# Kernel tuning notes

Hardware: AMD Instinct MI355X
Metric: run time of the kernel (lower is better)

The kernel has to match this reference:

```python
import jax, jax.numpy as jnp
import numpy as np

W_BITS = 4  # active precision (max of supported_bits)
EPS = 0.005  # clamp margin from the original module


def _dequant_kbit(qweight, lut, w_bits):
    """Bit-plane LUT dequant.
    qweight: [w_bits, O, I//32] int32, plane b holds bit b (MSB-first code) of each
    weight's k-bit index, 32 consecutive input positions per int32 word (LSB-first
    within a word). lut: [O, 2**w_bits]. Returns dense weight [O, I].
    """
    O = qweight.shape[1]
    shifts = jnp.arange(32, dtype=jnp.int32)                     # bit position within word
    bits = (qweight[:, :, :, None] >> shifts) & 1                # [w_bits, O, I//32, 32]
    plane_w = (1 << (w_bits - 1 - jnp.arange(w_bits, dtype=jnp.int32)))
    idx = (bits * plane_w[:, None, None, None]).sum(axis=0)      # [O, I//32, 32]
    idx = idx.reshape(O, -1)                                     # [O, I]
    return jnp.take_along_axis(lut, idx, axis=1)                 # [O, I]


def _csr_dense(rows, cols, vals, O, I):
    """Scatter CSR (indptr=rows) into a dense [O, I] matrix."""
    nnz = cols.shape[0]
    k = jnp.arange(nnz, dtype=rows.dtype)
    row_ids = jnp.searchsorted(rows, k, side='right') - 1        # CSR row of each nnz
    return jnp.zeros((O, I), dtype=vals.dtype).at[row_ids, cols].add(vals)


def setup_inputs() -> dict:
    key = jax.random.key(0)
    ks = jax.random.split(key, 7)
    B, S, I, O = 4, 2048, 4096, 4096
    NNZ = 65536
    x = jax.random.normal(ks[0], (B, S, I), dtype=jnp.float32)
    qweight = jax.random.randint(ks[1], (W_BITS, O, I // 32), 0, 2147483647, dtype=jnp.int32)
    lut = jax.random.normal(ks[2], (O, 2 ** W_BITS), dtype=jnp.float32) * 0.05
    rows = jnp.sort(jax.random.randint(ks[3], (O + 1,), 0, NNZ, dtype=jnp.int32))
    rows = rows.at[0].set(0).at[-1].set(NNZ)                     # valid CSR indptr
    cols = jax.random.randint(ks[4], (NNZ,), 0, I, dtype=jnp.int32)
    vals = jax.random.normal(ks[5], (NNZ,), dtype=jnp.float32) * 0.01
    bias = jax.random.normal(ks[6], (O,), dtype=jnp.float32) * 0.01
    return {"x": x, "qweight": qweight, "lut": lut, "rows": rows,
            "cols": cols, "vals": vals, "bias": bias}


def reference(x, qweight, lut, rows, cols, vals, bias):
    O = qweight.shape[1]
    I = x.shape[-1]
    weight = _dequant_kbit(qweight, lut, W_BITS)                 # [O, I]
    y = jnp.einsum('bsi,oi->bso', x, weight)                     # dense quantized GEMM
    w_sp = _csr_dense(rows, cols, vals, O, I)                    # sparse outlier weights
    y = y + jnp.einsum('bsi,oi->bso', x, w_sp)
    y = y + bias
    fmax = jnp.finfo(x.dtype).max * (1.0 - EPS)
    return jnp.clip(y, -fmax, fmax)
```

## Files before the change

kernel.cpp:

```cpp
#include <hip/hip_runtime.h>
#include <stdint.h>

#define Mdim 8192
#define Ndim 4096
#define Kdim 4096

#define BM 256
#define BN 256
#define BK 32
#define NT (Kdim / BK)

typedef float f32x4 __attribute__((ext_vector_type(4)));
typedef __bf16 bf16x8 __attribute__((ext_vector_type(8)));
typedef unsigned short ushort_t;

#define FMAXC 3.3858093490333422e+38f

__device__ __forceinline__ ushort_t f2bf(float f) {
    unsigned u = __float_as_uint(f);
    u += 0x7fffu + ((u >> 16) & 1u);
    return (ushort_t)(u >> 16);
}

__device__ __forceinline__ void gload_lds16(const void* g, void* l) {
    __builtin_amdgcn_global_load_lds(
        (const __attribute__((address_space(1))) uint32_t*)g,
        (__attribute__((address_space(3))) uint32_t*)(uint32_t)(uintptr_t)l,
        16, 0, 0);
}

__global__ __launch_bounds__(128) void dequant_kernel(
        const int* __restrict__ qw, const float* __restrict__ lut,
        const int* __restrict__ rows, const int* __restrict__ cols,
        const float* __restrict__ vals, ushort_t* __restrict__ w16) {
    __shared__ float wrow[128 * 33];
    __shared__ float slut[16];
    const int o = blockIdx.x;
    const int t = threadIdx.x;

    if (t < 16) slut[t] = lut[o * 16 + t];
    __syncthreads();

    const int q0 = qw[0 * Ndim * 128 + o * 128 + t];
    const int q1 = qw[1 * Ndim * 128 + o * 128 + t];
    const int q2 = qw[2 * Ndim * 128 + o * 128 + t];
    const int q3 = qw[3 * Ndim * 128 + o * 128 + t];
    float* dst = &wrow[t * 33];
#pragma unroll
    for (int j = 0; j < 32; ++j) {
        int idx = (((q0 >> j) & 1) << 3) | (((q1 >> j) & 1) << 2) |
                  (((q2 >> j) & 1) << 1) | ((q3 >> j) & 1);
        dst[j] = slut[idx];
    }
    __syncthreads();

    const int beg = rows[o], end = rows[o + 1];
    for (int k = beg + t; k < end; k += 128) {
        int c = cols[k];
        atomicAdd(&wrow[c + (c >> 5)], vals[k]);
    }
    __syncthreads();

    __align__(16) ushort_t tmp[32];
#pragma unroll
    for (int j = 0; j < 32; ++j) tmp[j] = f2bf(dst[j]);
    uint4* dstg = (uint4*)(w16 + (size_t)o * Kdim + t * 32);
    const uint4* srcg = (const uint4*)tmp;
#pragma unroll
    for (int j = 0; j < 4; ++j) dstg[j] = srcg[j];
}

__global__ __launch_bounds__(256) void convx_kernel(
        const float* __restrict__ x, ushort_t* __restrict__ y) {
    size_t i = ((size_t)blockIdx.x * 256 + threadIdx.x) * 8;
    float4 a = *(const float4*)(x + i);
    float4 b = *(const float4*)(x + i + 4);
    __align__(16) ushort_t r[8] = {f2bf(a.x), f2bf(a.y), f2bf(a.z), f2bf(a.w),
                                   f2bf(b.x), f2bf(b.y), f2bf(b.z), f2bf(b.w)};
    *(uint4*)(y + i) = *(const uint4*)r;
}

__global__ __launch_bounds__(512, 2) void gemm_kernel(
        const ushort_t* __restrict__ A, const ushort_t* __restrict__ Bw,
        const float* __restrict__ bias, float* __restrict__ C) {
    __shared__ __align__(16) char lds[131072];

    const int wgid = blockIdx.x;
    const int swz = (wgid & 7) * 64 + (wgid >> 3);
    const int bn = swz & 15, bm = swz >> 4;
    const int m0 = bm * BM, n0 = bn * BN;

    const int tid = threadIdx.x;
    const int lane = tid & 63, wid = tid >> 6;
    const int wr = wid >> 2, wc = wid & 3;
    const int fr = lane & 15, kg = lane >> 4;

    const int sline = tid >> 3;
    const int slot = (tid & 7) ^ (sline & 7);
    const int srow0 = (sline << 1) + (slot >> 2);
    const int skel = (slot & 3) * 8;
    const ushort_t* gA = A + (size_t)(m0 + srow0) * Kdim + skel;
    const ushort_t* gB = Bw + (size_t)(n0 + srow0) * Kdim + skel;

    auto stageA = [&](int bufd, int t2) {
        const ushort_t* s = gA + (size_t)t2 * BK;
        char* d = lds + bufd * 16384 + tid * 16;
        gload_lds16(s, d);
        gload_lds16(s + (size_t)128 * Kdim, d + 8192);
    };
    auto stageB = [&](int bufd, int t2) {
        const ushort_t* s = gB + (size_t)t2 * BK;
        char* d = lds + 65536 + bufd * 16384 + tid * 16;
        gload_lds16(s, d);
        gload_lds16(s + (size_t)128 * Kdim, d + 8192);
    };

    const int offL = (fr >> 1) * 128 + (((((fr & 1) << 2) | kg) ^ (fr >> 1)) << 4);

    f32x4 acc[8][4];
#pragma unroll
    for (int i = 0; i < 8; ++i)
#pragma unroll
        for (int j = 0; j < 4; ++j) acc[i][j] = (f32x4){0.f, 0.f, 0.f, 0.f};

    stageA(0, 0); stageB(0, 0);
    stageA(1, 1); stageB(1, 1);
    asm volatile("s_waitcnt vmcnt(4)" ::: "memory");
    asm volatile("s_barrier" ::: "memory");

#pragma unroll 1
    for (int t = 0; t < NT; ++t) {
        const int bufi = t & 3;
        const int buf2 = (t + 2) & 3;
        const bool pf = (t + 2 < NT);
        const char* Ab = lds + bufi * 16384;
        const char* Bb = lds + 65536 + bufi * 16384;

        bf16x8 Af0[4], Bf[4];
#pragma unroll
        for (int m = 0; m < 4; ++m)
            Af0[m] = *(const bf16x8*)(Ab + wr * 8192 + m * 1024 + offL);
#pragma unroll
        for (int n = 0; n < 4; ++n)
            Bf[n] = *(const bf16x8*)(Bb + wc * 4096 + n * 1024 + offL);
        if (pf) stageA(buf2, t + 2);
        asm volatile("s_barrier" ::: "memory");
        asm volatile("s_waitcnt lgkmcnt(0)" ::: "memory");
        __builtin_amdgcn_s_setprio(1);
#pragma unroll
        for (int m = 0; m < 4; ++m)
#pragma unroll
            for (int n = 0; n < 4; ++n)
                acc[m][n] = __builtin_amdgcn_mfma_f32_16x16x32_bf16(
                    Af0[m], Bf[n], acc[m][n], 0, 0, 0);
        __builtin_amdgcn_s_setprio(0);
        asm volatile("s_barrier" ::: "memory");

        bf16x8 Af1[4];
#pragma unroll
        for (int m = 0; m < 4; ++m)
            Af1[m] = *(const bf16x8*)(Ab + wr * 8192 + (m + 4) * 1024 + offL);
        if (pf) stageB(buf2, t + 2);
        asm volatile("s_barrier" ::: "memory");
        asm volatile("s_waitcnt lgkmcnt(0)" ::: "memory");
        __builtin_amdgcn_s_setprio(1);
#pragma unroll
        for (int m = 0; m < 4; ++m)
#pragma unroll
            for (int n = 0; n < 4; ++n)
                acc[m + 4][n] = __builtin_amdgcn_mfma_f32_16x16x32_bf16(
                    Af1[m], Bf[n], acc[m + 4][n], 0, 0, 0);
        __builtin_amdgcn_s_setprio(0);
        if (t < NT - 2) {
            asm volatile("s_waitcnt vmcnt(4)" ::: "memory");
        } else if (t == NT - 2) {
            asm volatile("s_waitcnt vmcnt(0)" ::: "memory");
        }
        asm volatile("s_barrier" ::: "memory");
    }

    const int rg = lane >> 4;
#pragma unroll
    for (int nf = 0; nf < 4; ++nf) {
        const int col = n0 + wc * 64 + nf * 16 + fr;
        const float bv = bias[col];
#pragma unroll
        for (int mf = 0; mf < 8; ++mf) {
            const int row = m0 + wr * 128 + mf * 16 + rg * 4;
            float* outp = C + (size_t)row * Ndim + col;
#pragma unroll
            for (int j = 0; j < 4; ++j) {
                float v = acc[mf][nf][j] + bv;
                v = fminf(fmaxf(v, -FMAXC), FMAXC);
                outp[(size_t)j * Ndim] = v;
            }
        }
    }
}

extern "C" void kernel_launch(void* const* d_in, const int* in_sizes, int n_in,
                              void* d_out, int out_size, void* d_ws, size_t ws_size,
                              hipStream_t stream) {
    const float* x    = (const float*)d_in[0];
    const int*   qw   = (const int*)d_in[1];
    const float* lut  = (const float*)d_in[2];
    const int*   rows = (const int*)d_in[3];
    const int*   cols = (const int*)d_in[4];
    const float* vals = (const float*)d_in[5];
    const float* bias = (const float*)d_in[6];
    float* out = (float*)d_out;

    ushort_t* x16 = (ushort_t*)d_ws;
    ushort_t* w16 = x16 + (size_t)Mdim * Kdim;

    hipLaunchKernelGGL(dequant_kernel, dim3(Ndim), dim3(128), 0, stream,
                       qw, lut, rows, cols, vals, w16);
    hipLaunchKernelGGL(convx_kernel, dim3((Mdim * Kdim) / (256 * 8)), dim3(256), 0, stream,
                       x, x16);
    hipLaunchKernelGGL(gemm_kernel, dim3((Mdim / BM) * (Ndim / BN)), dim3(512), 0, stream,
                       x16, w16, bias, out);
}
```

Before: 301.6 us.

## Simplify GEMM main loop to one barrier phase with upfront prefetch

Restructures the GEMM K-loop. It issues both A and B global-to-LDS prefetches at the start of each iteration, loads all eight A fragments and four B fragments at once, and runs all 32 MFMAs in a single block. This drops the two mid-iteration barriers and the interleaved half-phases, and uses incrementing pointers instead of recomputed offsets. The goal is less barrier and sync overhead. In exchange it loses the fine-grained interleaving of LDS reads and MFMAs, and raises register pressure from holding more fragments.

```diff
diff --git a/kernel.cpp b/kernel.cpp
--- a/kernel.cpp
+++ b/kernel.cpp
@@ -102,29 +102,30 @@
     const ushort_t* gA = A + (size_t)(m0 + srow0) * Kdim + skel;
     const ushort_t* gB = Bw + (size_t)(n0 + srow0) * Kdim + skel;
 
-    auto stageA = [&](int bufd, int t2) {
-        const ushort_t* s = gA + (size_t)t2 * BK;
+    const int offL = (fr >> 1) * 128 + (((((fr & 1) << 2) | kg) ^ (fr >> 1)) << 4);
+
+    f32x4 acc[8][4];
+#pragma unroll
+    for (int i = 0; i < 8; ++i)
+#pragma unroll
+        for (int j = 0; j < 4; ++j) acc[i][j] = (f32x4){0.f, 0.f, 0.f, 0.f};
+
+    const ushort_t* pA = gA;
+    const ushort_t* pB = gB;
+
+    auto stageA = [&](int bufd) {
         char* d = lds + bufd * 16384 + tid * 16;
-        gload_lds16(s, d);
-        gload_lds16(s + (size_t)128 * Kdim, d + 8192);
+        gload_lds16(pA, d);
+        gload_lds16(pA + (size_t)128 * Kdim, d + 8192);
     };
-    auto stageB = [&](int bufd, int t2) {
-        const ushort_t* s = gB + (size_t)t2 * BK;
+    auto stageB = [&](int bufd) {
         char* d = lds + 65536 + bufd * 16384 + tid * 16;
-        gload_lds16(s, d);
-        gload_lds16(s + (size_t)128 * Kdim, d + 8192);
+        gload_lds16(pB, d);
+        gload_lds16(pB + (size_t)128 * Kdim, d + 8192);
     };
 
-    const int offL = (fr >> 1) * 128 + (((((fr & 1) << 2) | kg) ^ (fr >> 1)) << 4);
-
-    f32x4 acc[8][4];
-#pragma unroll
-    for (int i = 0; i < 8; ++i)
-#pragma unroll
-        for (int j = 0; j < 4; ++j) acc[i][j] = (f32x4){0.f, 0.f, 0.f, 0.f};
-
-    stageA(0, 0); stageB(0, 0);
-    stageA(1, 1); stageB(1, 1);
+    stageA(0); stageB(0); pA += BK; pB += BK;
+    stageA(1); stageB(1); pA += BK; pB += BK;
     asm volatile("s_waitcnt vmcnt(4)" ::: "memory");
     asm volatile("s_barrier" ::: "memory");
 
@@ -132,45 +133,40 @@
     for (int t = 0; t < NT; ++t) {
         const int bufi = t & 3;
         const int buf2 = (t + 2) & 3;
-        const bool pf = (t + 2 < NT);
         const char* Ab = lds + bufi * 16384;
         const char* Bb = lds + 65536 + bufi * 16384;
 
-        bf16x8 Af0[4], Bf[4];
-#pragma unroll
-        for (int m = 0; m < 4; ++m)
-            Af0[m] = *(const bf16x8*)(Ab + wr * 8192 + m * 1024 + offL);
-#pragma unroll
-        for (int n = 0; n < 4; ++n)
+        if (t + 2 < NT) {
+            stageA(buf2);
+            stageB(buf2);
+        }
+        pA += BK; pB += BK;
+
+        bf16x8 Af[8], Bf[4];
+#pragma unroll
+        for (int n = 0; n < 4; ++n) {
+            Af[n] = *(const bf16x8*)(Ab + wr * 8192 + n * 1024 + offL);
             Bf[n] = *(const bf16x8*)(Bb + wc * 4096 + n * 1024 + offL);
-        if (pf) stageA(buf2, t + 2);
-        asm volatile("s_barrier" ::: "memory");
-        asm volatile("s_waitcnt lgkmcnt(0)" ::: "memory");
+        }
+#pragma unroll
+        for (int m = 4; m < 8; ++m)
+            Af[m] = *(const bf16x8*)(Ab + wr * 8192 + m * 1024 + offL);
+
         __builtin_amdgcn_s_setprio(1);
 #pragma unroll
         for (int m = 0; m < 4; ++m)
 #pragma unroll
             for (int n = 0; n < 4; ++n)
                 acc[m][n] = __builtin_amdgcn_mfma_f32_16x16x32_bf16(
-                    Af0[m], Bf[n], acc[m][n], 0, 0, 0);
+                    Af[m], Bf[n], acc[m][n], 0, 0, 0);
+#pragma unroll
+        for (int m = 4; m < 8; ++m)
+#pragma unroll
+            for (int n = 0; n < 4; ++n)
+                acc[m][n] = __builtin_amdgcn_mfma_f32_16x16x32_bf16(
+                    Af[m], Bf[n], acc[m][n], 0, 0, 0);
         __builtin_amdgcn_s_setprio(0);
-        asm volatile("s_barrier" ::: "memory");
-
-        bf16x8 Af1[4];
-#pragma unroll
-        for (int m = 0; m < 4; ++m)
-            Af1[m] = *(const bf16x8*)(Ab + wr * 8192 + (m + 4) * 1024 + offL);
-        if (pf) stageB(buf2, t + 2);
-        asm volatile("s_barrier" ::: "memory");
-        asm volatile("s_waitcnt lgkmcnt(0)" ::: "memory");
-        __builtin_amdgcn_s_setprio(1);
-#pragma unroll
-        for (int m = 0; m < 4; ++m)
-#pragma unroll
-            for (int n = 0; n < 4; ++n)
-                acc[m + 4][n] = __builtin_amdgcn_mfma_f32_16x16x32_bf16(
-                    Af1[m], Bf[n], acc[m + 4][n], 0, 0, 0);
-        __builtin_amdgcn_s_setprio(0);
+
         if (t < NT - 2) {
             asm volatile("s_waitcnt vmcnt(4)" ::: "memory");
         } else if (t == NT - 2) {
```

Result: faster. 292.4 us (-3.0%).
